# Optimization experiments

Measured on AMD Instinct MI355X. Metric: run time of the kernel, lower is better.

The kernel has to match this reference:

```python
import jax, jax.numpy as jnp
import numpy as np

IMG, PATCH, DIM, DEPTH, HEADS = 224, 16, 768, 12, 12
GRID = IMG // PATCH            # 14 patches per side
NPATCH = GRID * GRID           # 196
N = NPATCH + 1                 # 197 tokens incl. cls
HD = DIM // HEADS              # 64
NRD = (2 * GRID - 1) ** 2 + 3  # 732 relative-distance entries (incl. 3 cls slots)
FF = 4 * DIM                   # 3072
BATCH = 32


def _rel_pos_index():
    # Faithful port of the torch buffer construction (with_cls_token=True).
    coords = np.stack(np.meshgrid(np.arange(GRID), np.arange(GRID), indexing='ij'))
    cf = coords.reshape(2, -1)                                   # [2, 196]
    rel = (cf[:, :, None] - cf[:, None, :]).transpose(1, 2, 0)   # [196,196,2]
    rel = rel.astype(np.int64)
    rel[:, :, 0] += GRID - 1
    rel[:, :, 1] += GRID - 1
    rel[:, :, 0] *= 2 * GRID - 1
    rpi = np.zeros((N, N), dtype=np.int32)
    rpi[1:, 1:] = rel.sum(-1)
    rpi[0, :] = NRD - 3
    rpi[:, 0] = NRD - 2
    rpi[0, 0] = NRD - 1
    return jnp.asarray(rpi)

RPI = _rel_pos_index()  # [197,197] int32, constant


def layernorm(x, w, b, eps=1e-5):
    mu = x.mean(-1, keepdims=True)
    var = x.var(-1, keepdims=True)  # biased, like torch LayerNorm
    return (x - mu) * jax.lax.rsqrt(var + eps) * w + b


def setup_inputs() -> dict:
    key = jax.random.key(0)
    ks = jax.random.split(key, 12)
    s = 0.02
    f32 = jnp.float32
    return {
        'x': jax.random.normal(ks[0], (BATCH, 3, IMG, IMG), f32),
        # PatchEmbed conv (stride == kernel) expressed as a matmul weight.
        'patch_w': jax.random.normal(ks[1], (DIM, 3 * PATCH * PATCH), f32) * s,
        'patch_b': jnp.zeros((DIM,), f32),
        'cls_token': jax.random.normal(ks[2], (1, 1, DIM), f32) * s,
        # Per-block params, stacked along depth for lax.scan.
        'norm1_w': jnp.ones((DEPTH, DIM), f32),
        'norm1_b': jnp.zeros((DEPTH, DIM), f32),
        'qkv_w': jax.random.normal(ks[3], (DEPTH, 3 * DIM, DIM), f32) * s,
        'q_bias': jax.random.normal(ks[4], (DEPTH, DIM), f32) * s,
        'v_bias': jax.random.normal(ks[5], (DEPTH, DIM), f32) * s,
        'rpb_table': jax.random.normal(ks[6], (DEPTH, NRD, HEADS), f32) * s,
        'proj_w': jax.random.normal(ks[7], (DEPTH, DIM, DIM), f32) * s,
        'proj_b': jnp.zeros((DEPTH, DIM), f32),
        'norm2_w': jnp.ones((DEPTH, DIM), f32),
        'norm2_b': jnp.zeros((DEPTH, DIM), f32),
        'fc1_w': jax.random.normal(ks[8], (DEPTH, FF, DIM), f32) * s,
        'fc1_b': jnp.zeros((DEPTH, FF), f32),
        'fc2_w': jax.random.normal(ks[9], (DEPTH, DIM, FF), f32) * s,
        'fc2_b': jnp.zeros((DEPTH, DIM), f32),
        'normf_w': jnp.ones((DIM,), f32),
        'normf_b': jnp.zeros((DIM,), f32),
    }


def reference(x, patch_w, patch_b, cls_token, norm1_w, norm1_b, qkv_w, q_bias, v_bias,
              rpb_table, proj_w, proj_b, norm2_w, norm2_b, fc1_w, fc1_b, fc2_w, fc2_b,
              normf_w, normf_b):
    B = x.shape[0]
    # Patch embed: stride==kernel conv == patchify + matmul.
    p = x.reshape(B, 3, GRID, PATCH, GRID, PATCH).transpose(0, 2, 4, 1, 3, 5)
    p = p.reshape(B, NPATCH, 3 * PATCH * PATCH)
    tokens = p @ patch_w.T + patch_b                              # [B,196,768]
    tokens = jnp.concatenate([jnp.broadcast_to(cls_token, (B, 1, DIM)), tokens], axis=1)
    scale = HD ** -0.5

    def block(h, params):
        (n1w, n1b, qw, qb, vb, rpt, pw, pb, n2w, n2b, f1w, f1b, f2w, f2b) = params
        y = layernorm(h, n1w, n1b)
        bias = jnp.concatenate([qb, jnp.zeros_like(vb), vb])      # k bias is zero
        qkv = (y @ qw.T + bias).reshape(B, N, 3, HEADS, HD).transpose(2, 0, 3, 1, 4)
        q, k, v = qkv[0] * scale, qkv[1], qkv[2]                  # [B,H,N,HD]
        attn = jnp.einsum('bhnd,bhmd->bhnm', q, k)                # [B,H,N,N]
        rpb = rpt[RPI]                                            # [N,N,H] gather
        attn = attn + rpb.transpose(2, 0, 1)[None]
        attn = jax.nn.softmax(attn, axis=-1)
        o = jnp.einsum('bhnm,bhmd->bnhd', attn, v).reshape(B, N, DIM)
        h = h + o @ pw.T + pb
        y = layernorm(h, n2w, n2b)
        y = jax.nn.gelu(y @ f1w.T + f1b, approximate=False)       # torch nn.GELU (erf)
        h = h + y @ f2w.T + f2b
        return h, None

    params = (norm1_w, norm1_b, qkv_w, q_bias, v_bias, rpb_table, proj_w, proj_b,
              norm2_w, norm2_b, fc1_w, fc1_b, fc2_w, fc2_b)
    tokens, _ = jax.lax.scan(block, tokens, params)
    return layernorm(tokens, normf_w, normf_b)                    # [B,197,768]
```

## Files before the change

### kernel.cpp

```cpp
#include <hip/hip_runtime.h>
#include <hip/hip_bf16.h>


#define B_     32
#define DIM_   768
#define N_     197
#define M_     (B_*N_)
#define NP_    196
#define MP_    (B_*NP_)
#define HEADS_ 12
#define HD_    64
#define FF_    3072
#define NRD_   732
#define QKV_   2304
#define DEPTH_ 12

typedef unsigned short u16;
typedef unsigned int   u32;
typedef __attribute__((ext_vector_type(4))) float    f32x4;
typedef __attribute__((ext_vector_type(8))) u16      ushort8;
typedef __attribute__((ext_vector_type(8))) __bf16   bf16x8;

__device__ __forceinline__ float b2f(u16 u) {
    return __builtin_bit_cast(float, ((u32)u) << 16);
}
__device__ __forceinline__ u16 f2b(float f) {
    u32 u = __builtin_bit_cast(u32, f);
    u32 r = u + 0x7fffu + ((u >> 16) & 1u);
    return (u16)(r >> 16);
}
__device__ __forceinline__ float lo16(u32 v) { return __builtin_bit_cast(float, v << 16); }
__device__ __forceinline__ float hi16(u32 v) { return __builtin_bit_cast(float, v & 0xffff0000u); }

__device__ __forceinline__ f32x4 mfma16(ushort8 a, ushort8 b, f32x4 c) {
    return __builtin_amdgcn_mfma_f32_16x16x32_bf16(
        __builtin_bit_cast(bf16x8, a), __builtin_bit_cast(bf16x8, b), c, 0, 0, 0);
}

__device__ __forceinline__ void gload16(const u16* g, u16* lds) {
    __builtin_amdgcn_global_load_lds(
        (const __attribute__((address_space(1))) void*)g,
        (__attribute__((address_space(3))) void*)lds, 16, 0, 0);
}

__device__ __forceinline__ float gelu_f(float x) {
    float z  = x * 0.70710678118654752f;
    float az = fabsf(z);
    float t  = 1.f / (1.f + 0.3275911f * az);
    float p  = t * (0.254829592f + t * (-0.284496736f + t * (1.421413741f +
               t * (-1.453152027f + t * 1.061405429f))));
    float er = 1.f - p * __expf(-az * az);
    er = __builtin_copysignf(er, z);
    return 0.5f * x * (1.f + er);
}

__global__ void cvt_k(const float* __restrict__ src, u16* __restrict__ dst, int n8) {
    int g = blockIdx.x * 256 + threadIdx.x;
    if (g >= n8) return;
    size_t o = (size_t)g * 8;
    float4 f0 = *(const float4*)(src + o);
    float4 f1 = *(const float4*)(src + o + 4);
    ushort8 r;
    r[0]=f2b(f0.x); r[1]=f2b(f0.y); r[2]=f2b(f0.z); r[3]=f2b(f0.w);
    r[4]=f2b(f1.x); r[5]=f2b(f1.y); r[6]=f2b(f1.z); r[7]=f2b(f1.w);
    *(ushort8*)(dst + o) = r;
}

#define SEG0 1769472
#define SEG1 589824
#define SEG2 2359296
#define SEG3 2359296
__global__ void cvt4_k(const float* __restrict__ s0, const float* __restrict__ s1,
                       const float* __restrict__ s2, const float* __restrict__ s3,
                       u16* __restrict__ dst) {
    int g = blockIdx.x * 256 + threadIdx.x;
    if (g >= (SEG0+SEG1+SEG2+SEG3)/8) return;
    size_t o = (size_t)g * 8;
    const float* src; size_t lo_;
    if (o < SEG0)             { src = s0; lo_ = o; }
    else if (o < SEG0+SEG1)   { src = s1; lo_ = o - SEG0; }
    else if (o < (size_t)SEG0+SEG1+SEG2) { src = s2; lo_ = o - SEG0 - SEG1; }
    else                      { src = s3; lo_ = o - SEG0 - SEG1 - SEG2; }
    float4 f0 = *(const float4*)(src + lo_);
    float4 f1 = *(const float4*)(src + lo_ + 4);
    ushort8 r;
    r[0]=f2b(f0.x); r[1]=f2b(f0.y); r[2]=f2b(f0.z); r[3]=f2b(f0.w);
    r[4]=f2b(f1.x); r[5]=f2b(f1.y); r[6]=f2b(f1.z); r[7]=f2b(f1.w);
    *(ushort8*)(dst + o) = r;
}

__global__ void patchify_k(const float* __restrict__ X, u16* __restrict__ P) {
    int idx = blockIdx.x * 256 + threadIdx.x;
    if (idx >= MP_ * DIM_) return;
    int row = idx / DIM_, k = idx - row * DIM_;
    int b = row / NP_, p = row - b * NP_;
    int gy = p / 14, gx = p - gy * 14;
    int c = k >> 8, r = k & 255;
    int py = r >> 4, px = r & 15;
    P[idx] = f2b(X[((b * 3 + c) * 224 + gy * 16 + py) * 224 + gx * 16 + px]);
}

__global__ void build_tokens_k(const float* __restrict__ P, const float* __restrict__ cls,
                               float* __restrict__ T) {
    int idx = blockIdx.x * 256 + threadIdx.x;
    if (idx >= M_ * DIM_) return;
    int row = idx / DIM_, c = idx - row * DIM_;
    int b = row / N_, t = row - b * N_;
    T[idx] = (t == 0) ? cls[c] : P[(size_t)(b * NP_ + t - 1) * DIM_ + c];
}

__global__ void qkvbias_all_k(const float* __restrict__ qb, const float* __restrict__ vb,
                              float* __restrict__ out) {
    int g = blockIdx.x * 256 + threadIdx.x;
    if (g >= DEPTH_ * QKV_) return;
    int l = g / QKV_, n = g - l * QKV_;
    out[g] = (n < DIM_) ? qb[l * DIM_ + n]
                        : (n < 2 * DIM_ ? 0.f : vb[l * DIM_ + n - 2 * DIM_]);
}

template <int OUTBF>
__global__ void layernorm_k(const float* __restrict__ X, const float* __restrict__ w,
                            const float* __restrict__ bta, void* __restrict__ Yv) {
    int row = blockIdx.x;
    const float* x = X + (size_t)row * DIM_;
    int t = threadIdx.x;
    float v[3]; float s = 0.f, q = 0.f;
#pragma unroll
    for (int i = 0; i < 3; i++) { float u = x[t + i * 256]; v[i] = u; s += u; q += u * u; }
#pragma unroll
    for (int off = 32; off > 0; off >>= 1) {
        s += __shfl_down(s, off, 64);
        q += __shfl_down(q, off, 64);
    }
    __shared__ float ss[4], qq[4];
    int wid = t >> 6, lane = t & 63;
    if (!lane) { ss[wid] = s; qq[wid] = q; }
    __syncthreads();
    s = ss[0] + ss[1] + ss[2] + ss[3];
    q = qq[0] + qq[1] + qq[2] + qq[3];
    float mu = s * (1.f / 768.f);
    float var = q * (1.f / 768.f) - mu * mu;
    float rs = rsqrtf(var + 1e-5f);
#pragma unroll
    for (int i = 0; i < 3; i++) {
        int c = t + i * 256;
        float o = (v[i] - mu) * rs * w[c] + bta[c];
        if (OUTBF) ((u16*)Yv)[(size_t)row * DIM_ + c] = f2b(o);
        else       ((float*)Yv)[(size_t)row * DIM_ + c] = o;
    }
}

template <int ACT, int OUTBF>
__launch_bounds__(512, 6)
__global__ void gemm_bt(const u16* __restrict__ A, const u16* __restrict__ W,
                        const float* __restrict__ bias, const float* res,
                        void* Cv, int M, int Nc, int K) {
    __shared__ __align__(16) u16 smem[6 * 4096];
    u16* As = smem;
    u16* Ws = smem + 3 * 4096;
    const int tid = threadIdx.x;
    const int lane = tid & 63, w = tid >> 6;
    const int llo = lane & 15, lhi = lane >> 4;
    const int wn = w & 1, wm = w >> 1;

    const int nwg = gridDim.x * gridDim.y;
    int bid = blockIdx.y * gridDim.x + blockIdx.x;
    {
        int q = nwg >> 3, r = nwg & 7;
        int xcd = bid & 7, idx = bid >> 3;
        bid = (xcd < r ? xcd * (q + 1) : r * (q + 1) + (xcd - r) * q) + idx;
    }
    const int m0 = (bid / gridDim.x) * 128, n0 = (bid % gridDim.x) * 128;

    f32x4 acc[2][4] = {};

    const int srow = tid >> 2;
    const int scol = ((tid & 3) ^ ((srow >> 1) & 3)) * 8;
    int ar = m0 + srow; if (ar >= M) ar = M - 1;
    const u16* ga = A + (size_t)ar * K + scol;
    const u16* gw = W + (size_t)(n0 + srow) * K + scol;
    const int ldso = (w * 16) * 32;

    const int rslot = (lhi ^ ((llo >> 1) & 3)) * 8;

    const int nt = K >> 5;

    gload16(ga,      As + ldso);
    gload16(gw,      Ws + ldso);
    gload16(ga + 32, As + 4096 + ldso);
    gload16(gw + 32, Ws + 4096 + ldso);

    int cbuf = 0, sbuf = 2;
    for (int t = 0; t < nt; ++t) {
        if (t < nt - 1) asm volatile("s_waitcnt vmcnt(2)" ::: "memory");
        else            asm volatile("s_waitcnt vmcnt(0)" ::: "memory");
        __builtin_amdgcn_s_barrier();

        const u16* ab = As + cbuf * 4096;
        const u16* wb = Ws + cbuf * 4096;
        ushort8 af[2], bfr[4];
#pragma unroll
        for (int mi = 0; mi < 2; mi++)
            af[mi] = *(const ushort8*)(ab + (wm * 32 + mi * 16 + llo) * 32 + rslot);
#pragma unroll
        for (int ni = 0; ni < 4; ni++)
            bfr[ni] = *(const ushort8*)(wb + (wn * 64 + ni * 16 + llo) * 32 + rslot);
#pragma unroll
        for (int mi = 0; mi < 2; mi++)
#pragma unroll
            for (int ni = 0; ni < 4; ni++)
                acc[mi][ni] = mfma16(af[mi], bfr[ni], acc[mi][ni]);

        if (t + 2 < nt) {
            gload16(ga + (size_t)(t + 2) * 32, As + sbuf * 4096 + ldso);
            gload16(gw + (size_t)(t + 2) * 32, Ws + sbuf * 4096 + ldso);
        }
        cbuf = (cbuf + 1 == 3) ? 0 : cbuf + 1;
        sbuf = (sbuf + 1 == 3) ? 0 : sbuf + 1;
    }

    __syncthreads();
    float* eb = (float*)smem;
#pragma unroll
    for (int half = 0; half < 2; ++half) {
        if (wn == half) {
#pragma unroll
            for (int mi = 0; mi < 2; mi++)
#pragma unroll
                for (int ni = 0; ni < 4; ni++)
#pragma unroll
                    for (int rg = 0; rg < 4; rg++)
                        eb[(wm * 32 + mi * 16 + lhi * 4 + rg) * 68 + ni * 16 + llo] =
                            acc[mi][ni][rg];
        }
        __syncthreads();
        if (OUTBF) {
#pragma unroll
            for (int i = 0; i < 2; ++i) {
                int idx = tid + i * 512;
                int row = idx >> 3, c8 = (idx & 7) * 8;
                int grow = m0 + row, gcol = n0 + half * 64 + c8;
                f32x4 v0 = *(const f32x4*)(eb + row * 68 + c8);
                f32x4 v1 = *(const f32x4*)(eb + row * 68 + c8 + 4);
                if (grow < M) {
                    float4 b0 = *(const float4*)(bias + gcol);
                    float4 b1 = *(const float4*)(bias + gcol + 4);
                    float o0[4] = {v0[0]+b0.x, v0[1]+b0.y, v0[2]+b0.z, v0[3]+b0.w};
                    float o1[4] = {v1[0]+b1.x, v1[1]+b1.y, v1[2]+b1.z, v1[3]+b1.w};
                    ushort8 r;
#pragma unroll
                    for (int j = 0; j < 4; j++) {
                        float a0 = ACT ? gelu_f(o0[j]) : o0[j];
                        float a1 = ACT ? gelu_f(o1[j]) : o1[j];
                        r[j] = f2b(a0); r[4 + j] = f2b(a1);
                    }
                    *(ushort8*)((u16*)Cv + (size_t)grow * Nc + gcol) = r;
                }
            }
        } else {
#pragma unroll
            for (int i = 0; i < 4; ++i) {
                int idx = tid + i * 512;
                int row = idx >> 4, c4 = (idx & 15) * 4;
                int grow = m0 + row, gcol = n0 + half * 64 + c4;
                f32x4 v = *(const f32x4*)(eb + row * 68 + c4);
                if (grow < M) {
                    float4 bv = *(const float4*)(bias + gcol);
                    float4 o;
                    o.x = v[0] + bv.x; o.y = v[1] + bv.y;
                    o.z = v[2] + bv.z; o.w = v[3] + bv.w;
                    if (ACT) { o.x = gelu_f(o.x); o.y = gelu_f(o.y);
                               o.z = gelu_f(o.z); o.w = gelu_f(o.w); }
                    if (res) {
                        float4 rv = *(const float4*)(res + (size_t)grow * Nc + gcol);
                        o.x += rv.x; o.y += rv.y; o.z += rv.z; o.w += rv.w;
                    }
                    *(float4*)((float*)Cv + (size_t)grow * Nc + gcol) = o;
                }
            }
        }
        __syncthreads();
    }
}

__device__ __forceinline__ int vswz(int d) {
    return ((d & 7) ^ ((d >> 3) & 7)) << 3;
}

__launch_bounds__(256)
__global__ void attn3_k(const u16* __restrict__ qkv, const float* __restrict__ rpt,
                        u16* __restrict__ O) {
    __shared__ u16 smem[16128 + 16384];
    u16* Ks = smem;
    u16* Vt = smem + 16128;
    u16* Ps = smem;
    const int b = blockIdx.x / HEADS_, hh = blockIdx.x % HEADS_;
    const int i0 = blockIdx.y * 64;
    const int t = threadIdx.x;
    const int w = t >> 6, lane = t & 63;
    const int lhi = lane >> 4, llo = lane & 15;
    const size_t base = (size_t)b * N_ * QKV_ + (size_t)hh * HD_;
    const int iw = i0 + w * 16;

    int qrow = iw + llo; if (qrow > 196) qrow = 196;
    const ushort8 af0 = *(const ushort8*)(qkv + base + (size_t)qrow * QKV_ + lhi * 8);
    const ushort8 af1 = *(const ushort8*)(qkv + base + (size_t)qrow * QKV_ + 32 + lhi * 8);

    for (int g = t; g < 1576; g += 256) {
        int j = g >> 3, d0 = (g & 7) * 8;
        ushort8 kv = *(const ushort8*)(qkv + base + (size_t)j * QKV_ + 768 + d0);
        *(ushort8*)(Ks + j * 72 + d0) = kv;
        ushort8 vv = *(const ushort8*)(qkv + base + (size_t)j * QKV_ + 1536 + d0);
#pragma unroll
        for (int e = 0; e < 8; e++) {
            int d = d0 + e;
            Vt[d * 256 + (j ^ vswz(d))] = ((const u16*)&vv)[e];
        }
    }
    if (t < 216) {
        int j = 197 + (t >> 3), d0 = (t & 7) * 8;
        *(uint4*)(Ks + j * 72 + d0) = make_uint4(0u, 0u, 0u, 0u);
    }
    for (int g = t; g < 1728; g += 256) {
        int d = g / 27, c = 197 + (g - d * 27);
        Vt[d * 256 + (c ^ vswz(d))] = 0;
    }
    __syncthreads();

    const bool wvalid = (iw <= 196);
    f32x4 acc[14] = {};
    float mx[4], sum[4];

    if (wvalid) {
#pragma unroll
        for (int jt = 0; jt < 14; jt++) {
            const u16* kp = Ks + (jt * 16 + llo) * 72 + lhi * 8;
            ushort8 b0 = *(const ushort8*)(kp);
            ushort8 b1 = *(const ushort8*)(kp + 32);
            acc[jt] = mfma16(af0, b0, acc[jt]);
            acc[jt] = mfma16(af1, b1, acc[jt]);
        }
        int iy4[4], ix4[4]; bool icls[4];
#pragma unroll
        for (int rg = 0; rg < 4; rg++) {
            int i = iw + lhi * 4 + rg; if (i > 196) i = 196;
            icls[rg] = (i == 0);
            int pi = i - 1;
            iy4[rg] = pi / 14; ix4[rg] = pi - iy4[rg] * 14;
            mx[rg] = -INFINITY;
        }
#pragma unroll
        for (int jt = 0; jt < 14; jt++) {
            int j = jt * 16 + llo;
            if (j <= 196) {
                bool jcls = (j == 0);
                int pj = j - 1;
                int jy = pj / 14, jx = pj - jy * 14;
#pragma unroll
                for (int rg = 0; rg < 4; rg++) {
                    int idx;
                    if (icls[rg])  idx = jcls ? (NRD_ - 1) : (NRD_ - 3);
                    else if (jcls) idx = NRD_ - 2;
                    else           idx = (iy4[rg] - jy + 13) * 27 + (ix4[rg] - jx + 13);
                    float sv = acc[jt][rg] * 0.125f + rpt[idx * HEADS_ + hh];
                    acc[jt][rg] = sv;
                    mx[rg] = fmaxf(mx[rg], sv);
                }
            } else {
#pragma unroll
                for (int rg = 0; rg < 4; rg++) acc[jt][rg] = -INFINITY;
            }
        }
#pragma unroll
        for (int rg = 0; rg < 4; rg++) {
#pragma unroll
            for (int off = 1; off < 16; off <<= 1)
                mx[rg] = fmaxf(mx[rg], __shfl_xor(mx[rg], off, 64));
            sum[rg] = 0.f;
        }
#pragma unroll
        for (int jt = 0; jt < 14; jt++)
#pragma unroll
            for (int rg = 0; rg < 4; rg++) {
                float ev = __expf(acc[jt][rg] - mx[rg]);
                acc[jt][rg] = ev;
                sum[rg] += ev;
            }
#pragma unroll
        for (int rg = 0; rg < 4; rg++) {
#pragma unroll
            for (int off = 1; off < 16; off <<= 1)
                sum[rg] += __shfl_xor(sum[rg], off, 64);
            sum[rg] = 1.f / sum[rg];
        }
#pragma unroll
        for (int jt = 0; jt < 14; jt++)
#pragma unroll
            for (int rg = 0; rg < 4; rg++) acc[jt][rg] *= sum[rg];
    }
    __syncthreads();

    if (wvalid) {
#pragma unroll
        for (int jt = 0; jt < 14; jt++)
#pragma unroll
            for (int rg = 0; rg < 4; rg++)
                Ps[(w * 16 + lhi * 4 + rg) * 232 + jt * 16 + llo] = f2b(acc[jt][rg]);
        f32x4 o[4] = {};
#pragma unroll
        for (int jk = 0; jk < 7; jk++) {
            ushort8 pa = *(const ushort8*)(Ps + (w * 16 + llo) * 232 + jk * 32 + lhi * 8);
#pragma unroll
            for (int dt = 0; dt < 4; dt++) {
                int d = dt * 16 + llo;
                ushort8 vf = *(const ushort8*)(Vt + d * 256 + ((jk * 32 + lhi * 8) ^ vswz(d)));
                o[dt] = mfma16(pa, vf, o[dt]);
            }
        }
#pragma unroll
        for (int dt = 0; dt < 4; dt++)
#pragma unroll
            for (int rg = 0; rg < 4; rg++) {
                int i = iw + lhi * 4 + rg;
                if (i <= 196)
                    O[(size_t)(b * N_ + i) * DIM_ + hh * HD_ + dt * 16 + llo] = f2b(o[dt][rg]);
            }
    }
}

extern "C" void kernel_launch(void* const* d_in, const int* in_sizes, int n_in,
                              void* d_out, int out_size, void* d_ws, size_t ws_size,
                              hipStream_t stream) {
    (void)in_sizes; (void)n_in; (void)out_size; (void)ws_size;
    const float* x    = (const float*)d_in[0];
    const float* pew  = (const float*)d_in[1];
    const float* peb  = (const float*)d_in[2];
    const float* cls  = (const float*)d_in[3];
    const float* n1w  = (const float*)d_in[4];
    const float* n1b  = (const float*)d_in[5];
    const float* qkvw = (const float*)d_in[6];
    const float* qb   = (const float*)d_in[7];
    const float* vb   = (const float*)d_in[8];
    const float* rpt  = (const float*)d_in[9];
    const float* pw   = (const float*)d_in[10];
    const float* pb   = (const float*)d_in[11];
    const float* n2w  = (const float*)d_in[12];
    const float* n2b  = (const float*)d_in[13];
    const float* f1w  = (const float*)d_in[14];
    const float* f1b  = (const float*)d_in[15];
    const float* f2w  = (const float*)d_in[16];
    const float* f2b_ = (const float*)d_in[17];
    const float* nfw  = (const float*)d_in[18];
    const float* nfb  = (const float*)d_in[19];

    float* ws = (float*)d_ws;
    float* h     = ws;
    u16*   y     = (u16*)(ws + 4841472);
    float* un    = ws + 4841472 + 2420736;
    u16*   wbuf  = (u16*)(un + 9682944);
    float* qbias = (float*)(wbuf + 7077888);
    u16*   qkvb   = (u16*)un;
    u16*   hidden = (u16*)un;
    u16*   pmat   = (u16*)un;
    float* pout   = un + 4816896;

    const int MT = (M_ + 127) / 128;

    cvt_k<<<288, 256, 0, stream>>>(pew, wbuf, SEG1 / 8);
    patchify_k<<<(MP_ * DIM_ + 255) / 256, 256, 0, stream>>>(x, pmat);
    qkvbias_all_k<<<(DEPTH_ * QKV_ + 255) / 256, 256, 0, stream>>>(qb, vb, qbias);
    gemm_bt<0, 0><<<dim3(6, 49), 512, 0, stream>>>(pmat, wbuf, peb, nullptr, pout,
                                                   MP_, DIM_, DIM_);
    build_tokens_k<<<(M_ * DIM_ + 255) / 256, 256, 0, stream>>>(pout, cls, h);

    for (int l = 0; l < 12; l++) {
        layernorm_k<1><<<M_, 256, 0, stream>>>(h, n1w + l * DIM_, n1b + l * DIM_, y);
        cvt4_k<<<3456, 256, 0, stream>>>(qkvw + (size_t)l * SEG0, pw + (size_t)l * SEG1,
                                         f1w + (size_t)l * SEG2, f2w + (size_t)l * SEG3, wbuf);
        gemm_bt<0, 1><<<dim3(18, MT), 512, 0, stream>>>(y, wbuf, qbias + l * QKV_, nullptr,
                                                        qkvb, M_, QKV_, DIM_);
        attn3_k<<<dim3(384, 4), 256, 0, stream>>>(qkvb, rpt + (size_t)l * NRD_ * HEADS_, y);
        gemm_bt<0, 0><<<dim3(6, MT), 512, 0, stream>>>(y, wbuf + SEG0, pb + l * DIM_, h, h,
                                                       M_, DIM_, DIM_);
        layernorm_k<1><<<M_, 256, 0, stream>>>(h, n2w + l * DIM_, n2b + l * DIM_, y);
        gemm_bt<1, 1><<<dim3(24, MT), 512, 0, stream>>>(y, wbuf + SEG0 + SEG1, f1b + l * FF_,
                                                        nullptr, hidden, M_, FF_, DIM_);
        gemm_bt<0, 0><<<dim3(6, MT), 512, 0, stream>>>(hidden, wbuf + SEG0 + SEG1 + SEG2,
                                                       f2b_ + l * DIM_, h, h, M_, DIM_, FF_);
    }
    layernorm_k<0><<<M_, 256, 0, stream>>>(h, nfw, nfb, d_out);
}
```

Baseline: 2.940 ms.

## Add 64-row GEMM tiles for narrow outputs and fuse token scatter into patch GEMM

Templates the GEMM on the M-tile size so the three 768-wide GEMMs (proj, fc2, patch embed) use 64-row tiles, roughly doubling block count to fill more CUs. With BM=64 only half the waves stage A tiles, and the epilogue writes the full 128-column tile in one pass. The patch-embedding GEMM now writes directly into the token buffer with a row remap that skips the cls slot, and a small kernel fills the cls rows, replacing the separate token-building copy. Smaller tiles reduce weight reuse per block and change the vmcnt wait logic per wave group.

```diff
diff --git a/kernel.cpp b/kernel.cpp
--- a/kernel.cpp
+++ b/kernel.cpp
@@ -100,13 +100,11 @@
     P[idx] = f2b(X[((b * 3 + c) * 224 + gy * 16 + py) * 224 + gx * 16 + px]);
 }
 
-__global__ void build_tokens_k(const float* __restrict__ P, const float* __restrict__ cls,
-                               float* __restrict__ T) {
+__global__ void cls_fill_k(const float* __restrict__ cls, float* __restrict__ T) {
     int idx = blockIdx.x * 256 + threadIdx.x;
-    if (idx >= M_ * DIM_) return;
-    int row = idx / DIM_, c = idx - row * DIM_;
-    int b = row / N_, t = row - b * N_;
-    T[idx] = (t == 0) ? cls[c] : P[(size_t)(b * NP_ + t - 1) * DIM_ + c];
+    if (idx >= B_ * DIM_) return;
+    int b = idx / DIM_, c = idx - b * DIM_;
+    T[(size_t)b * N_ * DIM_ + c] = cls[c];
 }
 
 __global__ void qkvbias_all_k(const float* __restrict__ qb, const float* __restrict__ vb,
@@ -150,18 +148,22 @@
     }
 }
 
-template <int ACT, int OUTBF>
+template <int ACT, int OUTBF, int BM_, int TOKMAP>
 __launch_bounds__(512, 6)
 __global__ void gemm_bt(const u16* __restrict__ A, const u16* __restrict__ W,
                         const float* __restrict__ bias, const float* res,
                         void* Cv, int M, int Nc, int K) {
-    __shared__ __align__(16) u16 smem[6 * 4096];
+    constexpr int NWN = (BM_ == 128) ? 2 : 4;
+    constexpr int NI  = 8 / NWN;
+    constexpr int ASZ = BM_ * 32;
+    constexpr int WSZ = 128 * 32;
+    __shared__ __align__(16) u16 smem[3 * (ASZ + WSZ)];
     u16* As = smem;
-    u16* Ws = smem + 3 * 4096;
+    u16* Ws = smem + 3 * ASZ;
     const int tid = threadIdx.x;
     const int lane = tid & 63, w = tid >> 6;
     const int llo = lane & 15, lhi = lane >> 4;
-    const int wn = w & 1, wm = w >> 1;
+    const int wn = w % NWN, wm = w / NWN;
 
     const int nwg = gridDim.x * gridDim.y;
     int bid = blockIdx.y * gridDim.x + blockIdx.x;
@@ -170,14 +172,14 @@
         int xcd = bid & 7, idx = bid >> 3;
         bid = (xcd < r ? xcd * (q + 1) : r * (q + 1) + (xcd - r) * q) + idx;
     }
-    const int m0 = (bid / gridDim.x) * 128, n0 = (bid % gridDim.x) * 128;
-
-    f32x4 acc[2][4] = {};
+    const int m0 = (bid / gridDim.x) * BM_, n0 = (bid % gridDim.x) * 128;
+
+    f32x4 acc[2][NI] = {};
 
     const int srow = tid >> 2;
     const int scol = ((tid & 3) ^ ((srow >> 1) & 3)) * 8;
-    int ar = m0 + srow; if (ar >= M) ar = M - 1;
-    const u16* ga = A + (size_t)ar * K + scol;
+    int arow = m0 + srow; if (arow >= M) arow = M - 1;
+    const u16* ga = A + (size_t)arow * K + scol;
     const u16* gw = W + (size_t)(n0 + srow) * K + scol;
     const int ldso = (w * 16) * 32;
 
@@ -185,64 +187,132 @@
 
     const int nt = K >> 5;
 
-    gload16(ga,      As + ldso);
-    gload16(gw,      Ws + ldso);
-    gload16(ga + 32, As + 4096 + ldso);
-    gload16(gw + 32, Ws + 4096 + ldso);
+    auto stage = [&](int tt, int bb) {
+        if (BM_ == 128 || w < 4)
+            gload16(ga + (size_t)tt * 32, As + bb * ASZ + ldso);
+        gload16(gw + (size_t)tt * 32, Ws + bb * WSZ + ldso);
+    };
+
+    stage(0, 0);
+    stage(1, 1);
 
     int cbuf = 0, sbuf = 2;
     for (int t = 0; t < nt; ++t) {
-        if (t < nt - 1) asm volatile("s_waitcnt vmcnt(2)" ::: "memory");
-        else            asm volatile("s_waitcnt vmcnt(0)" ::: "memory");
+        if (t < nt - 1) {
+            if constexpr (BM_ == 128) {
+                asm volatile("s_waitcnt vmcnt(2)" ::: "memory");
+            } else {
+                if (w < 4) asm volatile("s_waitcnt vmcnt(2)" ::: "memory");
+                else       asm volatile("s_waitcnt vmcnt(1)" ::: "memory");
+            }
+        } else {
+            asm volatile("s_waitcnt vmcnt(0)" ::: "memory");
+        }
         __builtin_amdgcn_s_barrier();
 
-        const u16* ab = As + cbuf * 4096;
-        const u16* wb = Ws + cbuf * 4096;
-        ushort8 af[2], bfr[4];
+        const u16* ab = As + cbuf * ASZ;
+        const u16* wb = Ws + cbuf * WSZ;
+        ushort8 af[2], bfr[NI];
 #pragma unroll
         for (int mi = 0; mi < 2; mi++)
             af[mi] = *(const ushort8*)(ab + (wm * 32 + mi * 16 + llo) * 32 + rslot);
 #pragma unroll
-        for (int ni = 0; ni < 4; ni++)
-            bfr[ni] = *(const ushort8*)(wb + (wn * 64 + ni * 16 + llo) * 32 + rslot);
+        for (int ni = 0; ni < NI; ni++)
+            bfr[ni] = *(const ushort8*)(wb + (wn * NI * 16 + ni * 16 + llo) * 32 + rslot);
 #pragma unroll
         for (int mi = 0; mi < 2; mi++)
 #pragma unroll
-            for (int ni = 0; ni < 4; ni++)
+            for (int ni = 0; ni < NI; ni++)
                 acc[mi][ni] = mfma16(af[mi], bfr[ni], acc[mi][ni]);
 
-        if (t + 2 < nt) {
-            gload16(ga + (size_t)(t + 2) * 32, As + sbuf * 4096 + ldso);
-            gload16(gw + (size_t)(t + 2) * 32, Ws + sbuf * 4096 + ldso);
-        }
+        if (t + 2 < nt) stage(t + 2, sbuf);
         cbuf = (cbuf + 1 == 3) ? 0 : cbuf + 1;
         sbuf = (sbuf + 1 == 3) ? 0 : sbuf + 1;
     }
 
     __syncthreads();
     float* eb = (float*)smem;
-#pragma unroll
-    for (int half = 0; half < 2; ++half) {
-        if (wn == half) {
-#pragma unroll
-            for (int mi = 0; mi < 2; mi++)
-#pragma unroll
-                for (int ni = 0; ni < 4; ni++)
-#pragma unroll
-                    for (int rg = 0; rg < 4; rg++)
-                        eb[(wm * 32 + mi * 16 + lhi * 4 + rg) * 68 + ni * 16 + llo] =
-                            acc[mi][ni][rg];
-        }
+    if constexpr (BM_ == 128) {
+#pragma unroll
+        for (int half = 0; half < 2; ++half) {
+            if (wn == half) {
+#pragma unroll
+                for (int mi = 0; mi < 2; mi++)
+#pragma unroll
+                    for (int ni = 0; ni < NI; ni++)
+#pragma unroll
+                        for (int rg = 0; rg < 4; rg++)
+                            eb[(wm * 32 + mi * 16 + lhi * 4 + rg) * 68 + ni * 16 + llo] =
+                                acc[mi][ni][rg];
+            }
+            __syncthreads();
+            if (OUTBF) {
+#pragma unroll
+                for (int i = 0; i < 2; ++i) {
+                    int idx = tid + i * 512;
+                    int row = idx >> 3, c8 = (idx & 7) * 8;
+                    int grow = m0 + row, gcol = n0 + half * 64 + c8;
+                    f32x4 v0 = *(const f32x4*)(eb + row * 68 + c8);
+                    f32x4 v1 = *(const f32x4*)(eb + row * 68 + c8 + 4);
+                    if (grow < M) {
+                        float4 b0 = *(const float4*)(bias + gcol);
+                        float4 b1 = *(const float4*)(bias + gcol + 4);
+                        float o0[4] = {v0[0]+b0.x, v0[1]+b0.y, v0[2]+b0.z, v0[3]+b0.w};
+                        float o1[4] = {v1[0]+b1.x, v1[1]+b1.y, v1[2]+b1.z, v1[3]+b1.w};
+                        ushort8 r;
+#pragma unroll
+                        for (int j = 0; j < 4; j++) {
+                            float a0 = ACT ? gelu_f(o0[j]) : o0[j];
+                            float a1 = ACT ? gelu_f(o1[j]) : o1[j];
+                            r[j] = f2b(a0); r[4 + j] = f2b(a1);
+                        }
+                        *(ushort8*)((u16*)Cv + (size_t)grow * Nc + gcol) = r;
+                    }
+                }
+            } else {
+#pragma unroll
+                for (int i = 0; i < 4; ++i) {
+                    int idx = tid + i * 512;
+                    int row = idx >> 4, c4 = (idx & 15) * 4;
+                    int grow = m0 + row, gcol = n0 + half * 64 + c4;
+                    f32x4 v = *(const f32x4*)(eb + row * 68 + c4);
+                    if (grow < M) {
+                        float4 bv = *(const float4*)(bias + gcol);
+                        float4 o;
+                        o.x = v[0] + bv.x; o.y = v[1] + bv.y;
+                        o.z = v[2] + bv.z; o.w = v[3] + bv.w;
+                        if (ACT) { o.x = gelu_f(o.x); o.y = gelu_f(o.y);
+                                   o.z = gelu_f(o.z); o.w = gelu_f(o.w); }
+                        if (res) {
+                            float4 rv = *(const float4*)(res + (size_t)grow * Nc + gcol);
+                            o.x += rv.x; o.y += rv.y; o.z += rv.z; o.w += rv.w;
+                        }
+                        *(float4*)((float*)Cv + (size_t)grow * Nc + gcol) = o;
+                    }
+                }
+            }
+            __syncthreads();
+        }
+    } else {
+#pragma unroll
+        for (int mi = 0; mi < 2; mi++)
+#pragma unroll
+            for (int ni = 0; ni < NI; ni++)
+#pragma unroll
+                for (int rg = 0; rg < 4; rg++)
+                    eb[(wm * 32 + mi * 16 + lhi * 4 + rg) * 132 +
+                       wn * NI * 16 + ni * 16 + llo] = acc[mi][ni][rg];
         __syncthreads();
         if (OUTBF) {
 #pragma unroll
             for (int i = 0; i < 2; ++i) {
                 int idx = tid + i * 512;
-                int row = idx >> 3, c8 = (idx & 7) * 8;
-                int grow = m0 + row, gcol = n0 + half * 64 + c8;
-                f32x4 v0 = *(const f32x4*)(eb + row * 68 + c8);
-                f32x4 v1 = *(const f32x4*)(eb + row * 68 + c8 + 4);
+                int row = idx >> 4, c8 = (idx & 15) * 8;
+                int grow = m0 + row, gcol = n0 + c8;
+                f32x4 v0 = *(const f32x4*)(eb + row * 132 + c8);
+                f32x4 v1 = *(const f32x4*)(eb + row * 132 + c8 + 4);
                 if (grow < M) {
+                    int orow = TOKMAP ? (grow + grow / 196 + 1) : grow;
                     float4 b0 = *(const float4*)(bias + gcol);
                     float4 b1 = *(const float4*)(bias + gcol + 4);
                     float o0[4] = {v0[0]+b0.x, v0[1]+b0.y, v0[2]+b0.z, v0[3]+b0.w};
@@ -254,17 +324,18 @@
                         float a1 = ACT ? gelu_f(o1[j]) : o1[j];
                         r[j] = f2b(a0); r[4 + j] = f2b(a1);
                     }
-                    *(ushort8*)((u16*)Cv + (size_t)grow * Nc + gcol) = r;
+                    *(ushort8*)((u16*)Cv + (size_t)orow * Nc + gcol) = r;
                 }
             }
         } else {
 #pragma unroll
             for (int i = 0; i < 4; ++i) {
                 int idx = tid + i * 512;
-                int row = idx >> 4, c4 = (idx & 15) * 4;
-                int grow = m0 + row, gcol = n0 + half * 64 + c4;
-                f32x4 v = *(const f32x4*)(eb + row * 68 + c4);
+                int row = idx >> 5, c4 = (idx & 31) * 4;
+                int grow = m0 + row, gcol = n0 + c4;
+                f32x4 v = *(const f32x4*)(eb + row * 132 + c4);
                 if (grow < M) {
+                    int orow = TOKMAP ? (grow + grow / 196 + 1) : grow;
                     float4 bv = *(const float4*)(bias + gcol);
                     float4 o;
                     o.x = v[0] + bv.x; o.y = v[1] + bv.y;
@@ -272,14 +343,13 @@
                     if (ACT) { o.x = gelu_f(o.x); o.y = gelu_f(o.y);
                                o.z = gelu_f(o.z); o.w = gelu_f(o.w); }
                     if (res) {
-                        float4 rv = *(const float4*)(res + (size_t)grow * Nc + gcol);
+                        float4 rv = *(const float4*)(res + (size_t)orow * Nc + gcol);
                         o.x += rv.x; o.y += rv.y; o.z += rv.z; o.w += rv.w;
                     }
-                    *(float4*)((float*)Cv + (size_t)grow * Nc + gcol) = o;
+                    *(float4*)((float*)Cv + (size_t)orow * Nc + gcol) = o;
                 }
             }
         }
-        __syncthreads();
     }
 }
 
@@ -462,31 +532,31 @@
     u16*   qkvb   = (u16*)un;
     u16*   hidden = (u16*)un;
     u16*   pmat   = (u16*)un;
-    float* pout   = un + 4816896;
-
-    const int MT = (M_ + 127) / 128;
 
     cvt_k<<<288, 256, 0, stream>>>(pew, wbuf, SEG1 / 8);
     patchify_k<<<(MP_ * DIM_ + 255) / 256, 256, 0, stream>>>(x, pmat);
     qkvbias_all_k<<<(DEPTH_ * QKV_ + 255) / 256, 256, 0, stream>>>(qb, vb, qbias);
-    gemm_bt<0, 0><<<dim3(6, 49), 512, 0, stream>>>(pmat, wbuf, peb, nullptr, pout,
-                                                   MP_, DIM_, DIM_);
-    build_tokens_k<<<(M_ * DIM_ + 255) / 256, 256, 0, stream>>>(pout, cls, h);
+    gemm_bt<0, 0, 64, 1><<<dim3(6, 98), 512, 0, stream>>>(pmat, wbuf, peb, nullptr, h,
+                                                          MP_, DIM_, DIM_);
+    cls_fill_k<<<(B_ * DIM_ + 255) / 256, 256, 0, stream>>>(cls, h);
 
     for (int l = 0; l < 12; l++) {
         layernorm_k<1><<<M_, 256, 0, stream>>>(h, n1w + l * DIM_, n1b + l * DIM_, y);
         cvt4_k<<<3456, 256, 0, stream>>>(qkvw + (size_t)l * SEG0, pw + (size_t)l * SEG1,
                                          f1w + (size_t)l * SEG2, f2w + (size_t)l * SEG3, wbuf);
-        gemm_bt<0, 1><<<dim3(18, MT), 512, 0, stream>>>(y, wbuf, qbias + l * QKV_, nullptr,
-                                                        qkvb, M_, QKV_, DIM_);
+        gemm_bt<0, 1, 128, 0><<<dim3(18, 50), 512, 0, stream>>>(y, wbuf, qbias + l * QKV_,
+                                                                nullptr, qkvb, M_, QKV_, DIM_);
         attn3_k<<<dim3(384, 4), 256, 0, stream>>>(qkvb, rpt + (size_t)l * NRD_ * HEADS_, y);
-        gemm_bt<0, 0><<<dim3(6, MT), 512, 0, stream>>>(y, wbuf + SEG0, pb + l * DIM_, h, h,
-                                                       M_, DIM_, DIM_);
+        gemm_bt<0, 0, 64, 0><<<dim3(6, 99), 512, 0, stream>>>(y, wbuf + SEG0, pb + l * DIM_,
+                                                              h, h, M_, DIM_, DIM_);
         layernorm_k<1><<<M_, 256, 0, stream>>>(h, n2w + l * DIM_, n2b + l * DIM_, y);
-        gemm_bt<1, 1><<<dim3(24, MT), 512, 0, stream>>>(y, wbuf + SEG0 + SEG1, f1b + l * FF_,
-                                                        nullptr, hidden, M_, FF_, DIM_);
-        gemm_bt<0, 0><<<dim3(6, MT), 512, 0, stream>>>(hidden, wbuf + SEG0 + SEG1 + SEG2,
-                                                       f2b_ + l * DIM_, h, h, M_, DIM_, FF_);
+        gemm_bt<1, 1, 128, 0><<<dim3(24, 50), 512, 0, stream>>>(y, wbuf + SEG0 + SEG1,
+                                                                f1b + l * FF_, nullptr,
+                                                                hidden, M_, FF_, DIM_);
+        gemm_bt<0, 0, 64, 0><<<dim3(6, 99), 512, 0, stream>>>(hidden,
+                                                              wbuf + SEG0 + SEG1 + SEG2,
+                                                              f2b_ + l * DIM_, h, h,
+                                                              M_, DIM_, FF_);
     }
     layernorm_k<0><<<M_, 256, 0, stream>>>(h, nfw, nfb, d_out);
 }
```

Result: slower. 3.061 ms (+4.1%).
